# Kernel optimization log

Measured on AMD Instinct MI355X. Metric: run time of the kernel, lower is better.

Reference implementation:

```python
import jax, jax.numpy as jnp
import numpy as np

PARENT_LIST = [0, 0, 1, 2, 3, 4, 5, 6, 7, 8, 8, 3, 11, 12, 13, 14, 15, 15, 0, 18, 19, 20, 0, 22, 23, 24, 3]
J, D, H, L, DFF = 27, 512, 8, 6, 2048
DH = D // H
RADIUS = 0.1
B, N = 64, 2048
NEG = -1e9  # large finite negative: exp underflows to exactly 0 in fp32, grad-safe


def _topo_mask():
    m = np.full((J, J), NEG, dtype=np.float32)
    for c, p in enumerate(PARENT_LIST):
        m[c, c] = 0.0
        if c != p:
            m[c, p] = 0.0
            m[p, c] = 0.0
    return jnp.asarray(m)


def _radius_scales():
    s = np.ones(J, dtype=np.float32)
    s[[0, 1, 2, 3, 18, 22]] = 0.6
    s[[9, 10, 16, 17, 20, 21, 24, 25, 26]] = 1.5
    return jnp.asarray(s).reshape(1, J, 1)


def _ln(x, s, b):
    mu = jnp.mean(x, -1, keepdims=True)
    v = jnp.mean((x - mu) ** 2, -1, keepdims=True)
    return (x - mu) * jax.lax.rsqrt(v + 1e-5) * s + b


def _mha(q_in, k_in, v_in, qkv_w, qkv_b, out_w, out_b, add_mask):
    Bq, Q, _ = q_in.shape
    S = k_in.shape[1]
    q = (q_in @ qkv_w[:, :D] + qkv_b[:D]).reshape(Bq, Q, H, DH)
    k = (k_in @ qkv_w[:, D:2 * D] + qkv_b[D:2 * D]).reshape(Bq, S, H, DH)
    v = (v_in @ qkv_w[:, 2 * D:] + qkv_b[2 * D:]).reshape(Bq, S, H, DH)
    scores = jnp.einsum('bqhd,bkhd->bhqk', q, k) * np.float32(1.0 / np.sqrt(DH))
    attn = jax.nn.softmax(scores + add_mask, axis=-1)
    o = jnp.einsum('bhqk,bkhd->bqhd', attn, v).reshape(Bq, Q, D)
    return o @ out_w + out_b


def setup_inputs() -> dict:
    key = jax.random.key(0)
    ks = iter(jax.random.split(key, 40))
    def w(shape, scale=0.02):
        return jax.random.normal(next(ks), shape, jnp.float32) * scale
    return dict(
        x_t=jax.random.normal(next(ks), (B, J, 3), jnp.float32),
        t=jax.random.uniform(next(ks), (B, 1), jnp.float32),
        coarse_pose=jax.random.normal(next(ks), (B, J, 3), jnp.float32),
        radar_pc=jax.random.normal(next(ks), (B, N, 6), jnp.float32),
        pc_w=w((6, D)), pc_b=jnp.zeros(D),
        coarse_w=w((3, D)), coarse_b=jnp.zeros(D),
        state_w=w((3, D)), state_b=jnp.zeros(D),
        jid_emb=w((J, D), 1.0),
        dop_w1=w((1, 64)), dop_b1=jnp.zeros(64),
        dop_w2=w((64, D)), dop_b2=jnp.zeros(D),
        time_w1=w((1, D)), time_b1=jnp.zeros(D),
        time_w2=w((D, D)), time_b2=jnp.zeros(D),
        mod_w1=w((D, 2 * D)), mod_b1=jnp.zeros(2 * D),
        mod_w2=w((2 * D, 2 * D)), mod_b2=jnp.zeros(2 * D),
        diff_w=w((2 * D, D)), diff_b=jnp.zeros(D),
        vel_w=w((D, 3)), vel_b=jnp.zeros(3),
        sa_qkv_w=w((L, D, 3 * D)), sa_qkv_b=jnp.zeros((L, 3 * D)),
        sa_out_w=w((L, D, D)), sa_out_b=jnp.zeros((L, D)),
        ca_qkv_w=w((L, D, 3 * D)), ca_qkv_b=jnp.zeros((L, 3 * D)),
        ca_out_w=w((L, D, D)), ca_out_b=jnp.zeros((L, D)),
        ff1_w=w((L, D, DFF)), ff1_b=jnp.zeros((L, DFF)),
        ff2_w=w((L, DFF, D)), ff2_b=jnp.zeros((L, D)),
        ln1_s=jnp.ones((L, D)), ln1_b=jnp.zeros((L, D)),
        ln2_s=jnp.ones((L, D)), ln2_b=jnp.zeros((L, D)),
        ln3_s=jnp.ones((L, D)), ln3_b=jnp.zeros((L, D)),
    )


def reference(x_t, t, coarse_pose, radar_pc, pc_w, pc_b, coarse_w, coarse_b,
              state_w, state_b, jid_emb, dop_w1, dop_b1, dop_w2, dop_b2,
              time_w1, time_b1, time_w2, time_b2, mod_w1, mod_b1, mod_w2, mod_b2,
              diff_w, diff_b, vel_w, vel_b,
              sa_qkv_w, sa_qkv_b, sa_out_w, sa_out_b,
              ca_qkv_w, ca_qkv_b, ca_out_w, ca_out_b,
              ff1_w, ff1_b, ff2_w, ff2_b,
              ln1_s, ln1_b, ln2_s, ln2_b, ln3_s, ln3_b):
    p_idx = jnp.asarray(PARENT_LIST)
    topo = _topo_mask()          # [J,J] additive
    scales = _radius_scales()    # [1,J,1]
    pc_xyz = radar_pc[:, :, :3]
    pc_dop = radar_pc[:, :, 3:4]
    raw_memory = radar_pc @ pc_w + pc_b                               # [B,N,D]
    # euclidean distance via norm expansion (cdist p=2)
    d2 = (jnp.sum(x_t ** 2, -1)[:, :, None] + jnp.sum(pc_xyz ** 2, -1)[:, None, :]
          - 2.0 * jnp.einsum('bjc,bnc->bjn', x_t, pc_xyz))
    dist = jnp.sqrt(jnp.maximum(d2, 0.0))                             # [B,J,N]
    ar = scales * RADIUS                                              # [1,J,1]
    sig = ar / 2.0
    dw = jnp.exp(-dist ** 2 / (2.0 * sig ** 2))                       # [B,J,N]
    pi = jnp.max(dw, axis=1, keepdims=True)                           # [B,1,N]
    memory = raw_memory * jnp.swapaxes(pi, 1, 2)                      # [B,N,D]
    dop_feat = jax.nn.silu(pc_dop @ dop_w1 + dop_b1) @ dop_w2 + dop_b2
    denom = jnp.sum(dw, -1, keepdims=True) + 1e-6
    h_dop = jnp.einsum('bjn,bnd->bjd', dw, dop_feat) / denom
    h_coarse = coarse_pose @ coarse_w + coarse_b
    h_time = (jax.nn.silu(t @ time_w1 + time_b1) @ time_w2 + time_b2)[:, None, :]
    h_state = x_t @ state_w + state_b
    h_parent = h_state[:, p_idx, :]
    h_struct = jnp.concatenate([h_state, h_parent], -1) @ diff_w + diff_b
    query = h_coarse + h_time + h_dop + h_state + h_struct + jid_emb[None]
    mod = jax.nn.silu(h_state @ mod_w1 + mod_b1) @ mod_w2 + mod_b2
    shift, scale = jnp.split(mod, 2, axis=-1)
    query = query * (1.0 + scale) + shift
    # radius mask with nearest-point rescue
    smask = dist > ar
    min_idx = jnp.argmin(dist, axis=-1)                               # [B,J]
    rescue = jnp.arange(dist.shape[-1])[None, None, :] != min_idx[:, :, None]
    smask = jnp.where(jnp.all(smask, -1, keepdims=True), rescue, smask)
    mem_bias = jnp.where(smask, NEG, 0.0)[:, None, :, :]              # [B,1,J,N]
    tgt_bias = topo[None, None]                                       # [1,1,J,J]
    x = query
    for l in range(L):  # norm_first TransformerDecoderLayer, relu FFN, no dropout
        h = _ln(x, ln1_s[l], ln1_b[l])
        x = x + _mha(h, h, h, sa_qkv_w[l], sa_qkv_b[l], sa_out_w[l], sa_out_b[l], tgt_bias)
        h = _ln(x, ln2_s[l], ln2_b[l])
        x = x + _mha(h, memory, memory, ca_qkv_w[l], ca_qkv_b[l], ca_out_w[l], ca_out_b[l], mem_bias)
        h = _ln(x, ln3_s[l], ln3_b[l])
        x = x + jax.nn.relu(h @ ff1_w[l] + ff1_b[l]) @ ff2_w[l] + ff2_b[l]
    return x @ vel_w + vel_b
```

## Files before the change

kernel.cpp:

```cpp
#include <hip/hip_runtime.h>

#define J 27
#define D 512
#define H 8
#define DH 64
#define NLAYER 6
#define DFF 2048
#define NB 64
#define NP 2048
#define CAP 128
#define GCH 16
#define GPTS 128
#define NEGF -1000000000.0f

typedef unsigned short u16;
typedef __attribute__((ext_vector_type(8))) __bf16 bf16x8;
typedef __attribute__((ext_vector_type(4))) float f32x4;

__constant__ int c_parent[J] = {0,0,1,2,3,4,5,6,7,8,8,3,11,12,13,14,15,15,0,18,19,20,0,22,23,24,3};
__constant__ float c_scale[J] = {0.6f,0.6f,0.6f,0.6f,1.f,1.f,1.f,1.f,1.f,1.5f,1.5f,1.f,1.f,1.f,1.f,1.f,
                                 1.5f,1.5f,0.6f,1.f,1.5f,1.5f,0.6f,1.f,1.5f,1.5f,1.5f};

__device__ __forceinline__ float siluf(float x){ return x/(1.f+expf(-x)); }

__device__ __forceinline__ u16 f2bf(float f){
  union { float f; unsigned u; } x; x.f = f;
  unsigned r = x.u + 0x7FFFu + ((x.u >> 16) & 1u);
  return (u16)(r >> 16);
}
__device__ __forceinline__ float bf2f(u16 h){
  union { unsigned u; float f; } x; x.u = ((unsigned)h) << 16; return x.f;
}
__device__ __forceinline__ void csplit(float v, u16 &h, u16 &l){
  h = f2bf(v);
  l = f2bf(v - bf2f(h));
}

__global__ void k_perj(const float* __restrict__ x_t, const float* __restrict__ pc,
                       float* __restrict__ denom_sum, int* __restrict__ rescue,
                       int* __restrict__ allm, unsigned int* __restrict__ bitmap){
  int bj = blockIdx.x; int b = bj / J, j = bj % J;
  int t = threadIdx.x;
  float x0 = x_t[(b*J+j)*3+0];
  float x1 = x_t[(b*J+j)*3+1];
  float x2 = x_t[(b*J+j)*3+2];
  float sx = x0*x0+x1*x1+x2*x2;
  float ar = c_scale[j]*0.1f;
  float sig = ar*0.5f;
  float twos2 = 2.f*sig*sig;
  float sum = 0.f, bmin = 3.4e38f; int bidx = NP; int any = 0;
  for (int n = t; n < NP; n += 256){
    const float* p = pc + ((size_t)b*NP + n)*6;
    float p0=p[0], p1=p[1], p2=p[2];
    float d2 = sx + (p0*p0+p1*p1+p2*p2) - 2.f*(x0*p0+x1*p1+x2*p2);
    float dist = sqrtf(fmaxf(d2, 0.f));
    sum += expf(-(dist*dist)/twos2);
    if (dist < bmin){ bmin = dist; bidx = n; }
    if (dist <= ar){ any = 1; atomicOr(&bitmap[b*(NP/32)+(n>>5)], 1u<<(n&31)); }
// ... 37 lines not shown
      base++;
    }
  }
  if (t == 0) act_cnt[b] = total > CAP ? CAP : total;
}

__global__ void k_scan(const int* __restrict__ act_cnt, int* __restrict__ act_off,
                       int* __restrict__ act_total){
  if (threadIdx.x == 0){
    int s = 0;
    for (int b = 0; b < NB; ++b){ act_off[b] = s; s += act_cnt[b]; }
    act_total[0] = s;
  }
}

__launch_bounds__(256)
__global__ void k_gpart(const float* __restrict__ x_t, const float* __restrict__ pc,
                        const float* __restrict__ dop_w1, const float* __restrict__ dop_b1,
                        float* __restrict__ Gp){
  int b = blockIdx.x, ch = blockIdx.y; int t = threadIdx.x;
  __shared__ float sx[J*3];
  __shared__ float w1s[64], b1s[64];
  __shared__ float spx[GPTS], spy[GPTS], spz[GPTS], sdp[GPTS];
  __shared__ float hid[GPTS*65];
  __shared__ float dws[J*129];
  if (t < J*3) sx[t] = x_t[b*J*3 + t];
  if (t < 64){ w1s[t] = dop_w1[t]; b1s[t] = dop_b1[t]; }
  int n0 = ch*GPTS;
  if (t < GPTS){
    const float* p = pc + ((size_t)b*NP + n0 + t)*6;
    float2 f0 = *(const float2*)p;
    float2 f1 = *(const float2*)(p+2);
    spx[t]=f0.x; spy[t]=f0.y; spz[t]=f1.x; sdp[t]=f1.y;
  }
  __syncthreads();
  {
    int p = t>>1, h0 = (t&1)*32;
    float dop = sdp[p];
    #pragma unroll 8
    for (int i = 0; i < 32; ++i){
      int h = h0 + i;
      hid[p*65+h] = siluf(dop*w1s[h]+b1s[h]);
    }
  }
  for (int e = t; e < J*GPTS; e += 256){
    int j = e>>7, p = e&127;
    float x0=sx[j*3], x1=sx[j*3+1], x2=sx[j*3+2];
    float p0=spx[p], p1=spy[p], p2=spz[p];
    float d2 = (x0*x0+x1*x1+x2*x2) + (p0*p0+p1*p1+p2*p2) - 2.f*(x0*p0+x1*p1+x2*p2);
    float dist = sqrtf(fmaxf(d2, 0.f));
    float sig = c_scale[j]*0.05f;
    dws[j*129+p] = expf(-(dist*dist)/(2.f*sig*sig));
  }
  __syncthreads();
  int h = t & 63, jb = t >> 6;
  float acc[7] = {0.f,0.f,0.f,0.f,0.f,0.f,0.f};
  for (int p = 0; p < GPTS; ++p){
    float hv = hid[p*65+h];
    #pragma unroll
    for (int i = 0; i < 7; ++i){
      int j = jb + 4*i;
      if (j < J) acc[i] += dws[j*129+p]*hv;
    }
  }
  float* out = Gp + ((size_t)(b*GCH+ch))*J*64;
  #pragma unroll
  for (int i = 0; i < 7; ++i){
    int j = jb + 4*i;
    if (j < J) out[j*64+h] = acc[i];
  }
}

__global__ void k_gred(const float* __restrict__ Gp, float* __restrict__ G){
  int idx = blockIdx.x*256 + threadIdx.x;
  int bj = idx >> 6, h = idx & 63;
  int b = bj / J, j = bj % J;
  float s = 0.f;
  #pragma unroll
  for (int c = 0; c < GCH; ++c) s += Gp[((size_t)(b*GCH+c)*J + j)*64 + h];
  G[idx] = s;
}

__launch_bounds__(256)
__global__ void k_hdop2(const float* __restrict__ G, const float* __restrict__ dop_w2,
                        const float* __restrict__ dop_b2, const float* __restrict__ denom_sum,
                        float* __restrict__ h_dop){
  int b = blockIdx.x, half = blockIdx.y;
  int t = threadIdx.x;
  int d = half*256 + t;
  __shared__ float sG[J*64];
  __shared__ float sS[J], sI[J];
  for (int e = t; e < J*64; e += 256) sG[e] = G[(size_t)b*J*64 + e];
  if (t < J){ float S = denom_sum[b*J+t]; sS[t] = S; sI[t] = 1.f/(S+1e-6f); }
  __syncthreads();
  float acc[J];
  #pragma unroll
  for (int j = 0; j < J; ++j) acc[j] = 0.f;
  for (int h = 0; h < 64; ++h){
    float wv = dop_w2[h*D + d];
    #pragma unroll
    for (int j = 0; j < J; ++j) acc[j] += sG[j*64+h]*wv;
  }
  float b2 = dop_b2[d];
  #pragma unroll
  for (int j = 0; j < J; ++j)
    h_dop[(size_t)(b*J+j)*D + d] = (acc[j] + sS[j]*b2)*sI[j];
}

__global__ void k_stage1(const float* __restrict__ x_t, const float* __restrict__ state_w,
                         const float* __restrict__ state_b,
                         const float* __restrict__ coarse, const float* __restrict__ coarse_w,
                         const float* __restrict__ coarse_b,
                         const float* __restrict__ t_in, const float* __restrict__ time_w1,
                         const float* __restrict__ time_b1,
                         float* __restrict__ h_state, u16* __restrict__ hsh, u16* __restrict__ hsl,
                         float* __restrict__ h_coarse, u16* __restrict__ thh, u16* __restrict__ thl){
  const int RD = NB*J*D;
  int idx = blockIdx.x*256 + threadIdx.x;
  if (idx < RD){
    int r = idx / D, d = idx % D;
    const float* ir = x_t + r*3;
    float v = ir[0]*state_w[d] + ir[1]*state_w[D+d] + ir[2]*state_w[2*D+d] + state_b[d];
    h_state[idx] = v;
    u16 h,l; csplit(v,h,l); hsh[idx]=h; hsl[idx]=l;
  } else if (idx < 2*RD){
    int k = idx - RD;
    int r = k / D, d = k % D;
    const float* ir = coarse + r*3;
    h_coarse[k] = ir[0]*coarse_w[d] + ir[1]*coarse_w[D+d] + ir[2]*coarse_w[2*D+d] + coarse_b[d];
  } else if (idx < 2*RD + NB*D){
    int k = idx - 2*RD;
    int b = k / D, d = k % D;
    float v = siluf(t_in[b]*time_w1[d] + time_b1[d]);
    u16 h,l; csplit(v,h,l); thh[k]=h; thl[k]=l;
  }
}

__global__ void k_hs2(const float* __restrict__ h_state, u16* __restrict__ oh, u16* __restrict__ ol){
  int idx = blockIdx.x*256 + threadIdx.x;
  if (idx >= NB*J*2*D) return;
  int r = idx / (2*D), c = idx % (2*D);
  int b = r / J, j = r % J;
  float v;
  if (c < D) v = h_state[(size_t)r*D + c];
  else       v = h_state[((size_t)(b*J) + c_parent[j])*D + (c-D)];
  u16 h,l; csplit(v,h,l); oh[idx]=h; ol[idx]=l;
}

__global__ void k_query(const float* __restrict__ h_coarse, const float* __restrict__ h_time,
                        const float* __restrict__ h_dop, const float* __restrict__ h_state,
                        const float* __restrict__ hstruct, const float* __restrict__ jid,
                        const float* __restrict__ mod2, float* __restrict__ x){
  int idx = blockIdx.x*256 + threadIdx.x;
  if (idx >= NB*J*D) return;
  int r = idx / D, d = idx % D;
  int b = r / J, j = r % J;
  float q = h_coarse[idx] + h_time[b*D+d] + h_dop[idx] + h_state[idx] + hstruct[idx] + jid[j*D+d];
  float shift = mod2[(size_t)r*2*D + d];
  float scale = mod2[(size_t)r*2*D + D + d];
  x[idx] = q*(1.f+scale) + shift;
}

__global__ void k_memact(const float* __restrict__ x_t, const float* __restrict__ pc,
                         const float* __restrict__ pc_w, const float* __restrict__ pc_b,
                         const int* __restrict__ act_idx, const int* __restrict__ act_cnt,
                         const int* __restrict__ act_off, u16* __restrict__ mh, u16* __restrict__ ml){
  int b = blockIdx.x / CAP, i = blockIdx.x % CAP;
  if (i >= act_cnt[b]) return;
  int n = act_idx[b*CAP+i];
  int t = threadIdx.x;
  __shared__ float sdw[J];
  __shared__ float spi;
  const float* p = pc + ((size_t)b*NP+n)*6;
  if (t < J){
    float x0 = x_t[(b*J+t)*3+0], x1 = x_t[(b*J+t)*3+1], x2 = x_t[(b*J+t)*3+2];
    float p0=p[0], p1=p[1], p2=p[2];
    float d2 = (x0*x0+x1*x1+x2*x2) + (p0*p0+p1*p1+p2*p2) - 2.f*(x0*p0+x1*p1+x2*p2);
    float dist = sqrtf(fmaxf(d2,0.f));
    float sig = c_scale[t]*0.05f;
    sdw[t] = expf(-(dist*dist)/(2.f*sig*sig));
  }
  __syncthreads();
  if (t == 0){ float m = sdw[0]; for (int k = 1; k < J; ++k) m = fmaxf(m, sdw[k]); spi = m; }
  __syncthreads();
  float pi = spi;
  float p0=p[0],p1=p[1],p2=p[2],p3=p[3],p4=p[4],p5=p[5];
  int g = act_off[b] + i;
  for (int d = t; d < D; d += 128){
    float acc = pc_b[d] + p0*pc_w[d] + p1*pc_w[D+d] + p2*pc_w[2*D+d]
              + p3*pc_w[3*D+d] + p4*pc_w[4*D+d] + p5*pc_w[5*D+d];
    float v = acc * pi;
    u16 h,l; csplit(v,h,l);
    mh[(size_t)g*D + d] = h; ml[(size_t)g*D + d] = l;
  }
}

__launch_bounds__(256)
__global__ void k_wconv(const float* __restrict__ W, u16* __restrict__ Wt, int K, int N){
  int k0 = blockIdx.x*64, n0 = blockIdx.y*64;
  size_t zo = (size_t)blockIdx.z*K*N;
  __shared__ float tile[64][65];
  int t = threadIdx.x;
  #pragma unroll
  for (int i = 0; i < 16; ++i){
    int idx = i*256 + t; int k = idx>>6, n = idx&63;
    tile[k][n] = W[zo + (size_t)(k0+k)*N + n0+n];
  }
  __syncthreads();
  #pragma unroll
  for (int i = 0; i < 8; ++i){
    int idx = i*256 + t; int n = idx>>5, kp = (idx&31)*2;
    unsigned pk = (unsigned)f2bf(tile[kp][n]) | ((unsigned)f2bf(tile[kp+1][n])<<16);
    *(unsigned*)&Wt[zo + (size_t)(n0+n)*K + k0+kp] = pk;
  }
}

template<int TM>
__launch_bounds__(256)
__global__ void k_gemm(const u16* __restrict__ Agh, const u16* __restrict__ Agl,
                       const u16* __restrict__ Bt,
                       const float* __restrict__ bias, const float* __restrict__ res,
                       float* __restrict__ Cf, u16* __restrict__ Ch, u16* __restrict__ Cl,
                       int M, int N, int K, int act,
                       const int* __restrict__ Mdev, int ntx){
  int Meff = Mdev ? *Mdev : M;
  int nwg = gridDim.x;
  int q8 = nwg>>3, r8 = nwg&7;
  int xcd = blockIdx.x&7, loc = blockIdx.x>>3;
  int wg = (xcd < r8 ? xcd*(q8+1) : r8*(q8+1)+(xcd-r8)*q8) + loc;
  int row0 = (wg % ntx)*TM, col0 = (wg / ntx)*64;
  if (row0 >= Meff) return;

  constexpr int MFR = TM/32;
  constexpr int RW  = TM/2;
  __shared__ u16 sAh[TM*64], sAl[TM*64], sBh[64*64];
  int t = threadIdx.x;
  int lane = t&63, w = t>>6, wr = w>>1, wc = w&1;
  int sm = t>>3, kc = t&7;
  const u16* pAh1 = Agh + (size_t)(row0+sm)*K + kc*8;
  const u16* pAl1 = Agl + (size_t)(row0+sm)*K + kc*8;
  const u16* pAh2 = (TM==64) ? Agh + (size_t)(row0+sm+32)*K + kc*8 : pAh1;
  const u16* pAl2 = (TM==64) ? Agl + (size_t)(row0+sm+32)*K + kc*8 : pAl1;
  const u16* pB1 = Bt + (size_t)(col0+sm)*K + kc*8;
  const u16* pB2 = Bt + (size_t)(col0+sm+32)*K + kc*8;
  int o1 = (sm*128 + kc*16) ^ ((sm&7)<<4);
  int o2 = ((sm+32)*128 + kc*16) ^ ((sm&7)<<4);
  uint4 ra1, rl1, ra2, rl2, rb1, rb2;
  auto gload = [&](int kt){
    ra1 = *(const uint4*)(pAh1 + kt);
    rl1 = *(const uint4*)(pAl1 + kt);
    if constexpr (TM==64){
      ra2 = *(const uint4*)(pAh2 + kt);
      rl2 = *(const uint4*)(pAl2 + kt);
    }
    rb1 = *(const uint4*)(pB1 + kt);
    rb2 = *(const uint4*)(pB2 + kt);
  };
  auto stage = [&](){
    *(uint4*)((char*)sAh + o1) = ra1;
    *(uint4*)((char*)sAl + o1) = rl1;
    if constexpr (TM==64){
      *(uint4*)((char*)sAh + o2) = ra2;
      *(uint4*)((char*)sAl + o2) = rl2;
    }
    *(uint4*)((char*)sBh + o1) = rb1;
    *(uint4*)((char*)sBh + o2) = rb2;
  };
  int fr = lane&15, fkb = (lane>>4)*16;
  f32x4 acc[MFR][2] = {};
  gload(0);
  stage();
  __syncthreads();
  for (int kt = 0; kt < K; kt += 64){
    bool nxt = kt + 64 < K;
    if (nxt) gload(kt + 64);
    #pragma unroll
    for (int kk = 0; kk < 2; ++kk){
      bf16x8 ah[MFR], al[MFR], bh[2];
      #pragma unroll
      for (int m = 0; m < MFR; ++m){
        int row = wr*RW + m*16 + fr;
        int adr = (row*128 + kk*64 + fkb) ^ ((row&7)<<4);
        ah[m] = *(const bf16x8*)((char*)sAh + adr);
        al[m] = *(const bf16x8*)((char*)sAl + adr);
      }
      #pragma unroll
      for (int n = 0; n < 2; ++n){
        int rowb = wc*32 + n*16 + fr;
        int adr = (rowb*128 + kk*64 + fkb) ^ ((rowb&7)<<4);
        bh[n] = *(const bf16x8*)((char*)sBh + adr);
      }
      #pragma unroll
      for (int m = 0; m < MFR; ++m)
        #pragma unroll
        for (int n = 0; n < 2; ++n){
          acc[m][n] = __builtin_amdgcn_mfma_f32_16x16x32_bf16(al[m], bh[n], acc[m][n], 0,0,0);
          acc[m][n] = __builtin_amdgcn_mfma_f32_16x16x32_bf16(ah[m], bh[n], acc[m][n], 0,0,0);
        }
    }
    if (nxt){
      __syncthreads();
      stage();
      __syncthreads();
    }
  }
  int er = (lane>>4)*4, ec = lane&15;
  #pragma unroll
  for (int m = 0; m < MFR; ++m){
    #pragma unroll
    for (int qq = 0; qq < 4; ++qq){
      int r = row0 + wr*RW + m*16 + er + qq;
      if (r >= Meff) continue;
      #pragma unroll
      for (int n = 0; n < 2; ++n){
        int c = col0 + wc*32 + n*16 + ec;
        float v = acc[m][n][qq] + bias[c];
        if (res) v += res[(size_t)r*N + c];
        if (act == 1) v = v/(1.f+expf(-v));
        else if (act == 2) v = fmaxf(v, 0.f);
        if (Cf) Cf[(size_t)r*N + c] = v;
        if (Ch){
          u16 hh, ll; csplit(v, hh, ll);
          Ch[(size_t)r*N + c] = hh;
          Cl[(size_t)r*N + c] = ll;
        }
      }
    }
  }
}

__global__ void k_ln(const float* __restrict__ x, const float* __restrict__ s,
                     const float* __restrict__ bb, u16* __restrict__ oh, u16* __restrict__ ol){
  int r = blockIdx.x; int t = threadIdx.x;
  const float* xr = x + (size_t)r*D;
  float v0 = xr[t], v1 = xr[t+256];
  __shared__ float red[256];
  red[t] = v0+v1; __syncthreads();
  for (int st = 128; st > 0; st >>= 1){ if (t < st) red[t] += red[t+st]; __syncthreads(); }
  float mu = red[0]/(float)D;
  __syncthreads();
  float d0 = v0-mu, d1 = v1-mu;
  red[t] = d0*d0 + d1*d1; __syncthreads();
  for (int st = 128; st > 0; st >>= 1){ if (t < st) red[t] += red[t+st]; __syncthreads(); }
  float var = red[0]/(float)D;
  float rs = rsqrtf(var + 1e-5f);
  float y0 = d0*rs*s[t] + bb[t];
  float y1 = d1*rs*s[t+256] + bb[t+256];
  u16 h,l;
  csplit(y0,h,l); oh[(size_t)r*D+t]=h;     ol[(size_t)r*D+t]=l;
  csplit(y1,h,l); oh[(size_t)r*D+t+256]=h; ol[(size_t)r*D+t+256]=l;
}

__launch_bounds__(256)
__global__ void k_selfattn(const float* __restrict__ qkv, u16* __restrict__ oh, u16* __restrict__ ol){
  int bh = blockIdx.x; int b = bh / H, h = bh % H;
  int t = threadIdx.x;
  __shared__ float qs[J*DH], ks[J*DH], vs[J*DH];
  __shared__ float ss[J*J];
  for (int e = t; e < J*DH; e += 256){
    int j = e/DH, d = e%DH;
    const float* base = qkv + (size_t)(b*J+j)*1536 + h*DH + d;
    qs[e] = base[0]; ks[e] = base[512]; vs[e] = base[1024];
  }
  __syncthreads();
  for (int e = t; e < J*J; e += 256){
    int qj = e/J, kk = e%J;
    float acc = 0.f;
    for (int d = 0; d < DH; ++d) acc += qs[qj*DH+d]*ks[kk*DH+d];
    float bias = (qj==kk || c_parent[qj]==kk || c_parent[kk]==qj) ? 0.f : NEGF;
    ss[e] = acc*0.125f + bias;
  }
  __syncthreads();
  if (t < J){
    float m = -3.4e38f;
    for (int k = 0; k < J; ++k) m = fmaxf(m, ss[t*J+k]);
    float sum = 0.f;
    for (int k = 0; k < J; ++k){ float e_ = expf(ss[t*J+k]-m); ss[t*J+k] = e_; sum += e_; }
    float inv = 1.f/sum;
    for (int k = 0; k < J; ++k) ss[t*J+k] *= inv;
  }
  __syncthreads();
  for (int e = t; e < J*DH; e += 256){
    int j = e/DH, d = e%DH;
    float acc = 0.f;
    for (int k = 0; k < J; ++k) acc += ss[j*J+k]*vs[k*DH+d];
    u16 hh,ll; csplit(acc,hh,ll);
    oh[(size_t)(b*J+j)*D + h*DH + d] = hh;
    ol[(size_t)(b*J+j)*D + h*DH + d] = ll;
  }
}

__launch_bounds__(256)
__global__ void k_crossattn(const float* __restrict__ qbuf, const float* __restrict__ kv_act,
                            const float* __restrict__ x_t, const float* __restrict__ pc,
                            const int* __restrict__ act_idx, const int* __restrict__ act_cnt,
                            const int* __restrict__ act_off, const int* __restrict__ rescue,
                            const int* __restrict__ allm, u16* __restrict__ oh, u16* __restrict__ ol){
  int bh = blockIdx.x; int b = bh / H, h = bh % H;
  int t = threadIdx.x;
  int cnt = act_cnt[b], off = act_off[b];
  __shared__ float qs[J*DH];
  __shared__ float ks[CAP*DH];
  __shared__ float pxyz[CAP*3];
  __shared__ float sx[J*3];
  __shared__ int sn[CAP];
  __shared__ float ss[J*CAP];
  if (t < J*3) sx[t] = x_t[b*J*3+t];
  for (int e = t; e < J*DH; e += 256)
    qs[e] = qbuf[(size_t)(b*J + e/DH)*D + h*DH + (e%DH)];
  for (int e = t; e < cnt*DH; e += 256){
    int i = e/DH, d = e%DH;
    ks[e] = kv_act[(size_t)(off+i)*1024 + h*DH + d];
  }
  for (int i = t; i < cnt; i += 256){
    int n = act_idx[b*CAP+i]; sn[i] = n;
    const float* p = pc + ((size_t)b*NP+n)*6;
    pxyz[i*3] = p[0]; pxyz[i*3+1] = p[1]; pxyz[i*3+2] = p[2];
  }
  __syncthreads();
  for (int e = t; e < J*cnt; e += 256){
// ... 7 lines not shown
      float p0=pxyz[i*3], p1=pxyz[i*3+1], p2=pxyz[i*3+2];
      float d2 = (x0*x0+x1*x1+x2*x2) + (p0*p0+p1*p1+p2*p2) - 2.f*(x0*p0+x1*p1+x2*p2);
      float dist = sqrtf(fmaxf(d2,0.f));
      float ar = c_scale[j]*0.1f;
      bias = (dist > ar) ? NEGF : 0.f;
    }
    ss[j*CAP+i] = acc*0.125f + bias;
  }
  __syncthreads();
  if (t < J){
    float m = -3.4e38f;
    for (int i = 0; i < cnt; ++i) m = fmaxf(m, ss[t*CAP+i]);
    float sum = 0.f;
    for (int i = 0; i < cnt; ++i){ float e_ = expf(ss[t*CAP+i]-m); ss[t*CAP+i] = e_; sum += e_; }
    float inv = 1.f/sum;
    for (int i = 0; i < cnt; ++i) ss[t*CAP+i] *= inv;
  }
  __syncthreads();
  for (int e = t; e < J*DH; e += 256){
    int j = e/DH, d = e%DH;
    float acc = 0.f;
    for (int i = 0; i < cnt; ++i)
      acc += ss[j*CAP+i]*kv_act[(size_t)(off+i)*1024 + 512 + h*DH + d];
    u16 hh,ll; csplit(acc,hh,ll);
    oh[(size_t)(b*J+j)*D + h*DH + d] = hh;
    ol[(size_t)(b*J+j)*D + h*DH + d] = ll;
  }
}

__global__ void k_vel(const float* __restrict__ x, const float* __restrict__ vel_w,
                      const float* __restrict__ vel_b, float* __restrict__ out){
  int r = blockIdx.x; int t = threadIdx.x;
  int c = t >> 6; int lane = t & 63;
  float acc = 0.f;
  const float* xr = x + (size_t)r*D;
  for (int d = lane; d < D; d += 64) acc += xr[d]*vel_w[d*3+c];
  for (int s = 32; s > 0; s >>= 1) acc += __shfl_down(acc, s);
  if (lane == 0) out[r*3+c] = acc + vel_b[c];
}

static void gemm(const u16* Ah, const u16* Al, const u16* Bt, const float* bias,
                 const float* res, float* Cf, u16* Ch, u16* Cl,
                 int M, int N, int K, int act, const int* Mdev, int tm, hipStream_t s){
  if (tm == 32){
    int ntx = (M + 31) / 32;
    k_gemm<32><<<ntx*(N/64), 256, 0, s>>>(Ah, Al, Bt, bias, res, Cf, Ch, Cl, M, N, K, act, Mdev, ntx);
  } else {
    int ntx = (M + 63) / 64;
    k_gemm<64><<<ntx*(N/64), 256, 0, s>>>(Ah, Al, Bt, bias, res, Cf, Ch, Cl, M, N, K, act, Mdev, ntx);
  }
}

extern "C" void kernel_launch(void* const* d_in, const int* in_sizes, int n_in,
                              void* d_out, int out_size, void* d_ws, size_t ws_size,
                              hipStream_t stream){
  const float* x_t        = (const float*)d_in[0];
  const float* t_in       = (const float*)d_in[1];
  const float* coarse     = (const float*)d_in[2];
  const float* radar      = (const float*)d_in[3];
  const float* pc_w       = (const float*)d_in[4];
  const float* pc_b       = (const float*)d_in[5];
  const float* coarse_w   = (const float*)d_in[6];
  const float* coarse_b   = (const float*)d_in[7];
  const float* state_w    = (const float*)d_in[8];
  const float* state_b    = (const float*)d_in[9];
  const float* jid_emb    = (const float*)d_in[10];
  const float* dop_w1     = (const float*)d_in[11];
  const float* dop_b1     = (const float*)d_in[12];
  const float* dop_w2     = (const float*)d_in[13];
  const float* dop_b2     = (const float*)d_in[14];
  const float* time_w1    = (const float*)d_in[15];
  const float* time_b1    = (const float*)d_in[16];
// ... 36 lines not shown
    return r;
  };
  float*        denom_sum = (float*)alloc(R*4);
  int*          rescue    = (int*)  alloc(R*4);
  int*          allm      = (int*)  alloc(R*4);
  unsigned int* bitmap    = (unsigned int*)alloc(NB*(NP/32)*4);
  int*          act_idx   = (int*)  alloc(NB*CAP*4);
  int*          act_cnt   = (int*)  alloc(NB*4);
  int*          act_off   = (int*)  alloc(NB*4);
  int*          act_total = (int*)  alloc(64);
  float* Gp       = (float*)alloc((size_t)NB*GCH*J*64*4);
  float* G        = (float*)alloc((size_t)R*64*4);
  float* h_dop    = (float*)alloc((size_t)R*D*4);
  float* h_state  = (float*)alloc((size_t)R*D*4);
  float* h_coarse = (float*)alloc((size_t)R*D*4);
  float* hstruct  = (float*)alloc((size_t)R*D*4);
  float* xres     = (float*)alloc((size_t)R*D*4);
  float* qbuf     = (float*)alloc((size_t)R*D*4);
  float* h_time   = (float*)alloc((size_t)NB*D*4);
  float* mod2     = (float*)alloc((size_t)R*2*D*4);
  float* qkv      = (float*)alloc((size_t)R*3*D*4);
  float* kv_act   = (float*)alloc((size_t)NB*CAP*2*D*4);
  u16* hsh   = (u16*)alloc((size_t)R*D*2);
  u16* hsl   = (u16*)alloc((size_t)R*D*2);
  u16* hbufh = (u16*)alloc((size_t)R*D*2);
  u16* hbufl = (u16*)alloc((size_t)R*D*2);
  u16* attnoh= (u16*)alloc((size_t)R*D*2);
  u16* attnol= (u16*)alloc((size_t)R*D*2);
  u16* ffhh  = (u16*)alloc((size_t)R*DFF*2);
  u16* ffhl  = (u16*)alloc((size_t)R*DFF*2);
  u16* mah   = (u16*)alloc((size_t)NB*CAP*D*2);
  u16* mal   = (u16*)alloc((size_t)NB*CAP*D*2);
  u16* time_w2t = (u16*)alloc((size_t)512*512*2);
  u16* mod_w1t  = (u16*)alloc((size_t)1024*512*2);
  u16* mod_w2t  = (u16*)alloc((size_t)1024*1024*2);
  u16* diff_wt  = (u16*)alloc((size_t)512*1024*2);
  u16* sa_qkv_t = (u16*)alloc((size_t)NLAYER*1536*512*2);
  u16* sa_out_t = (u16*)alloc((size_t)NLAYER*512*512*2);
  u16* ca_qkv_t = (u16*)alloc((size_t)NLAYER*1536*512*2);
  u16* ca_out_t = (u16*)alloc((size_t)NLAYER*512*512*2);
  u16* ff1_t    = (u16*)alloc((size_t)NLAYER*2048*512*2);
  u16* ff2_t    = (u16*)alloc((size_t)NLAYER*512*2048*2);
  u16* thh   = attnoh;
  u16* thl   = attnol;
  u16* mod1h = ffhh;
  u16* mod1l = ffhl;
  u16* hs2h  = (u16*)kv_act;
  u16* hs2l  = (u16*)kv_act + (size_t)R*2*D;

  k_wconv<<<dim3(8, 8, 1),  256, 0, stream>>>(time_w2, time_w2t, 512, 512);
  k_wconv<<<dim3(8, 16, 1), 256, 0, stream>>>(mod_w1, mod_w1t, 512, 1024);
  k_wconv<<<dim3(16, 16, 1),256, 0, stream>>>(mod_w2, mod_w2t, 1024, 1024);
  k_wconv<<<dim3(16, 8, 1), 256, 0, stream>>>(diff_w, diff_wt, 1024, 512);
  k_wconv<<<dim3(8, 24, NLAYER), 256, 0, stream>>>(sa_qkv_w, sa_qkv_t, 512, 1536);
  k_wconv<<<dim3(8, 8, NLAYER),  256, 0, stream>>>(sa_out_w, sa_out_t, 512, 512);
  k_wconv<<<dim3(8, 24, NLAYER), 256, 0, stream>>>(ca_qkv_w, ca_qkv_t, 512, 1536);
  k_wconv<<<dim3(8, 8, NLAYER),  256, 0, stream>>>(ca_out_w, ca_out_t, 512, 512);
  k_wconv<<<dim3(8, 32, NLAYER), 256, 0, stream>>>(ff1_w, ff1_t, 512, 2048);
  k_wconv<<<dim3(32, 8, NLAYER), 256, 0, stream>>>(ff2_w, ff2_t, 2048, 512);

  hipMemsetAsync(bitmap, 0, NB*(NP/32)*4, stream);
  k_perj<<<R, 256, 0, stream>>>(x_t, radar, denom_sum, rescue, allm, bitmap);
  k_compact<<<NB, 64, 0, stream>>>(bitmap, act_idx, act_cnt);
  k_scan<<<1, 64, 0, stream>>>(act_cnt, act_off, act_total);
  k_gpart<<<dim3(NB, GCH), 256, 0, stream>>>(x_t, radar, dop_w1, dop_b1, Gp);
  k_gred<<<R*64/256, 256, 0, stream>>>(Gp, G);
  k_hdop2<<<dim3(NB, 2), 256, 0, stream>>>(G, dop_w2, dop_b2, denom_sum, h_dop);

  k_stage1<<<(2*R*D + NB*D + 255)/256, 256, 0, stream>>>(
      x_t, state_w, state_b, coarse, coarse_w, coarse_b, t_in, time_w1, time_b1,
      h_state, hsh, hsl, h_coarse, thh, thl);
  gemm(thh, thl, time_w2t, time_b2, nullptr, h_time, nullptr, nullptr, NB, 512, 512, 0, nullptr, 32, stream);
  gemm(hsh, hsl, mod_w1t, mod_b1, nullptr, nullptr, mod1h, mod1l, R, 1024, 512, 1, nullptr, 32, stream);
  gemm(mod1h, mod1l, mod_w2t, mod_b2, nullptr, mod2, nullptr, nullptr, R, 1024, 1024, 0, nullptr, 32, stream);
  k_hs2<<<(R*2*D+255)/256, 256, 0, stream>>>(h_state, hs2h, hs2l);
  gemm(hs2h, hs2l, diff_wt, diff_b, nullptr, hstruct, nullptr, nullptr, R, 512, 1024, 0, nullptr, 32, stream);
  k_query<<<(R*D+255)/256, 256, 0, stream>>>(h_coarse, h_time, h_dop, h_state, hstruct,
                                             jid_emb, mod2, xres);
  k_memact<<<NB*CAP, 128, 0, stream>>>(x_t, radar, pc_w, pc_b, act_idx, act_cnt, act_off, mah, mal);

  for (int l = 0; l < NLAYER; ++l){
    k_ln<<<R, 256, 0, stream>>>(xres, ln1_s + l*D, ln1_b + l*D, hbufh, hbufl);
    gemm(hbufh, hbufl, sa_qkv_t + (size_t)l*1536*512, sa_qkv_b + l*1536, nullptr,
         qkv, nullptr, nullptr, R, 1536, 512, 0, nullptr, 32, stream);
    k_selfattn<<<NB*H, 256, 0, stream>>>(qkv, attnoh, attnol);
    gemm(attnoh, attnol, sa_out_t + (size_t)l*512*512, sa_out_b + l*D, xres,
         xres, nullptr, nullptr, R, 512, 512, 0, nullptr, 32, stream);

    k_ln<<<R, 256, 0, stream>>>(xres, ln2_s + l*D, ln2_b + l*D, hbufh, hbufl);
    gemm(hbufh, hbufl, ca_qkv_t + (size_t)l*1536*512, ca_qkv_b + l*1536, nullptr,
         qbuf, nullptr, nullptr, R, 512, 512, 0, nullptr, 32, stream);
    gemm(mah, mal, ca_qkv_t + (size_t)l*1536*512 + (size_t)512*512, ca_qkv_b + l*1536 + 512,
         nullptr, kv_act, nullptr, nullptr, NB*CAP, 1024, 512, 0, act_total, 64, stream);
    k_crossattn<<<NB*H, 256, 0, stream>>>(qbuf, kv_act, x_t, radar, act_idx, act_cnt,
                                          act_off, rescue, allm, attnoh, attnol);
    gemm(attnoh, attnol, ca_out_t + (size_t)l*512*512, ca_out_b + l*D, xres,
         xres, nullptr, nullptr, R, 512, 512, 0, nullptr, 32, stream);

    k_ln<<<R, 256, 0, stream>>>(xres, ln3_s + l*D, ln3_b + l*D, hbufh, hbufl);
    gemm(hbufh, hbufl, ff1_t + (size_t)l*2048*512, ff1_b + l*DFF, nullptr,
         nullptr, ffhh, ffhl, R, 2048, 512, 2, nullptr, 32, stream);
    gemm(ffhh, ffhl, ff2_t + (size_t)l*512*2048, ff2_b + l*D, xres,
         xres, nullptr, nullptr, R, 512, 2048, 0, nullptr, 32, stream);
  }

  k_vel<<<R, 192, 0, stream>>>(xres, vel_w, vel_b, (float*)d_out);
}
```

Measured before the change: 1.217 ms.

## Drop split-bf16 activation compensation and use MFMA for doppler reduction

Activations were previously split into high and low bf16 halves, and every GEMM ran two MFMAs per tile to recover near-fp32 accuracy. This change keeps only the single bf16 value, which halves A-operand loads, shared memory and MFMA count, and removes the low-part buffers. The doppler weighted-sum kernel is also rewritten to use bf16 MFMA on swizzled shared tiles instead of a scalar FMA loop. Accuracy drops to plain bf16 for activations and for the Gaussian weights.

```diff
diff --git a/kernel.cpp b/kernel.cpp
--- a/kernel.cpp
+++ b/kernel.cpp
@@ -27,13 +27,6 @@
   union { float f; unsigned u; } x; x.f = f;
   unsigned r = x.u + 0x7FFFu + ((x.u >> 16) & 1u);
   return (u16)(r >> 16);
-}
-__device__ __forceinline__ float bf2f(u16 h){
-  union { unsigned u; float f; } x; x.u = ((unsigned)h) << 16; return x.f;
-}
-__device__ __forceinline__ void csplit(float v, u16 &h, u16 &l){
-  h = f2bf(v);
-  l = f2bf(v - bf2f(h));
 }
 
 __global__ void k_perj(const float* __restrict__ x_t, const float* __restrict__ pc,
@@ -117,8 +110,8 @@
   __shared__ float sx[J*3];
   __shared__ float w1s[64], b1s[64];
   __shared__ float spx[GPTS], spy[GPTS], spz[GPTS], sdp[GPTS];
-  __shared__ float hid[GPTS*65];
-  __shared__ float dws[J*129];
+  __shared__ u16 hidT[64*128];
+  __shared__ u16 dwsA[32*128];
   if (t < J*3) sx[t] = x_t[b*J*3 + t];
   if (t < 64){ w1s[t] = dop_w1[t]; b1s[t] = dop_b1[t]; }
   int n0 = ch*GPTS;
@@ -130,39 +123,73 @@
   }
   __syncthreads();
   {
-    int p = t>>1, h0 = (t&1)*32;
-    float dop = sdp[p];
-    #pragma unroll 8
-    for (int i = 0; i < 32; ++i){
-      int h = h0 + i;
-      hid[p*65+h] = siluf(dop*w1s[h]+b1s[h]);
-    }
-  }
-  for (int e = t; e < J*GPTS; e += 256){
-    int j = e>>7, p = e&127;
-    float x0=sx[j*3], x1=sx[j*3+1], x2=sx[j*3+2];
-    float p0=spx[p], p1=spy[p], p2=spz[p];
-    float d2 = (x0*x0+x1*x1+x2*x2) + (p0*p0+p1*p1+p2*p2) - 2.f*(x0*p0+x1*p1+x2*p2);
-    float dist = sqrtf(fmaxf(d2, 0.f));
-    float sig = c_scale[j]*0.05f;
-    dws[j*129+p] = expf(-(dist*dist)/(2.f*sig*sig));
-  }
-  __syncthreads();
-  int h = t & 63, jb = t >> 6;
-  float acc[7] = {0.f,0.f,0.f,0.f,0.f,0.f,0.f};
-  for (int p = 0; p < GPTS; ++p){
-    float hv = hid[p*65+h];
+    int h = t & 63, pb = (t>>6)*32;
+    float w1 = w1s[h], b1 = b1s[h];
+    char* base = (char*)hidT;
     #pragma unroll
-    for (int i = 0; i < 7; ++i){
-      int j = jb + 4*i;
-      if (j < J) acc[i] += dws[j*129+p]*hv;
+    for (int m = 0; m < 16; ++m){
+      float v0 = siluf(sdp[pb+2*m]*w1 + b1);
+      float v1 = siluf(sdp[pb+2*m+1]*w1 + b1);
+      unsigned pk = (unsigned)f2bf(v0) | ((unsigned)f2bf(v1) << 16);
+      int off = (h*256 + pb*2 + 4*m) ^ ((h&7)<<4);
+      *(unsigned*)(base + off) = pk;
+    }
+  }
+  {
+    int j = t & 31, pb = (t>>5)*16;
+    if (j < J){
+      float x0=sx[j*3], x1=sx[j*3+1], x2=sx[j*3+2];
+      float sxx = x0*x0+x1*x1+x2*x2;
+      float sig = c_scale[j]*0.05f;
+      float inv2 = 1.f/(2.f*sig*sig);
+      char* base = (char*)dwsA;
+      #pragma unroll
+      for (int m = 0; m < 8; ++m){
+        float v[2];
+        #pragma unroll
+        for (int u = 0; u < 2; ++u){
+          int p = pb + 2*m + u;
+          float p0=spx[p], p1=spy[p], p2=spz[p];
+          float d2 = sxx + (p0*p0+p1*p1+p2*p2) - 2.f*(x0*p0+x1*p1+x2*p2);
+          float dist = sqrtf(fmaxf(d2, 0.f));
+          v[u] = expf(-(dist*dist)*inv2);
+        }
+        unsigned pk = (unsigned)f2bf(v[0]) | ((unsigned)f2bf(v[1]) << 16);
+        int off = (j*256 + pb*2 + 4*m) ^ ((j&7)<<4);
+        *(unsigned*)(base + off) = pk;
+      }
+    }
+  }
+  __syncthreads();
+  int lane = t & 63, wv = t >> 6;
+  int h0 = wv * 16;
+  int fr = lane & 15, fkb = (lane>>4)*16;
+  f32x4 acc[2] = {};
+  #pragma unroll
+  for (int ks = 0; ks < 4; ++ks){
+    bf16x8 bfrag;
+    {
+      int row = h0 + fr;
+      int adr = (row*256 + ks*64 + fkb) ^ ((row&7)<<4);
+      bfrag = *(const bf16x8*)((char*)hidT + adr);
+    }
+    #pragma unroll
+    for (int m = 0; m < 2; ++m){
+      int row = m*16 + fr;
+      int adr = (row*256 + ks*64 + fkb) ^ ((row&7)<<4);
+      bf16x8 afrag = *(const bf16x8*)((char*)dwsA + adr);
+      acc[m] = __builtin_amdgcn_mfma_f32_16x16x32_bf16(afrag, bfrag, acc[m], 0,0,0);
     }
   }
   float* out = Gp + ((size_t)(b*GCH+ch))*J*64;
+  int er = (lane>>4)*4, ec = lane&15;
   #pragma unroll
-  for (int i = 0; i < 7; ++i){
-    int j = jb + 4*i;
-    if (j < J) out[j*64+h] = acc[i];
+  for (int m = 0; m < 2; ++m){
+    #pragma unroll
+    for (int q = 0; q < 4; ++q){
+      int j = m*16 + er + q;
+      if (j < J) out[j*64 + h0 + ec] = acc[m][q];
+    }
   }
 }
 
@@ -208,8 +235,8 @@
                          const float* __restrict__ coarse_b,
                          const float* __restrict__ t_in, const float* __restrict__ time_w1,
                          const float* __restrict__ time_b1,
-                         float* __restrict__ h_state, u16* __restrict__ hsh, u16* __restrict__ hsl,
-                         float* __restrict__ h_coarse, u16* __restrict__ thh, u16* __restrict__ thl){
+                         float* __restrict__ h_state, u16* __restrict__ hsh,
+                         float* __restrict__ h_coarse, u16* __restrict__ thh){
   const int RD = NB*J*D;
   int idx = blockIdx.x*256 + threadIdx.x;
   if (idx < RD){
@@ -217,7 +244,7 @@
     const float* ir = x_t + r*3;
     float v = ir[0]*state_w[d] + ir[1]*state_w[D+d] + ir[2]*state_w[2*D+d] + state_b[d];
     h_state[idx] = v;
-    u16 h,l; csplit(v,h,l); hsh[idx]=h; hsl[idx]=l;
+    hsh[idx] = f2bf(v);
   } else if (idx < 2*RD){
     int k = idx - RD;
     int r = k / D, d = k % D;
@@ -227,11 +254,11 @@
     int k = idx - 2*RD;
     int b = k / D, d = k % D;
     float v = siluf(t_in[b]*time_w1[d] + time_b1[d]);
-    u16 h,l; csplit(v,h,l); thh[k]=h; thl[k]=l;
-  }
-}
-
-__global__ void k_hs2(const float* __restrict__ h_state, u16* __restrict__ oh, u16* __restrict__ ol){
+    thh[k] = f2bf(v);
+  }
+}
+
+__global__ void k_hs2(const float* __restrict__ h_state, u16* __restrict__ oh){
   int idx = blockIdx.x*256 + threadIdx.x;
   if (idx >= NB*J*2*D) return;
   int r = idx / (2*D), c = idx % (2*D);
@@ -239,7 +266,7 @@
   float v;
   if (c < D) v = h_state[(size_t)r*D + c];
   else       v = h_state[((size_t)(b*J) + c_parent[j])*D + (c-D)];
-  u16 h,l; csplit(v,h,l); oh[idx]=h; ol[idx]=l;
+  oh[idx] = f2bf(v);
 }
 
 __global__ void k_query(const float* __restrict__ h_coarse, const float* __restrict__ h_time,
@@ -259,7 +286,7 @@
 __global__ void k_memact(const float* __restrict__ x_t, const float* __restrict__ pc,
                          const float* __restrict__ pc_w, const float* __restrict__ pc_b,
                          const int* __restrict__ act_idx, const int* __restrict__ act_cnt,
-                         const int* __restrict__ act_off, u16* __restrict__ mh, u16* __restrict__ ml){
+                         const int* __restrict__ act_off, u16* __restrict__ mh){
   int b = blockIdx.x / CAP, i = blockIdx.x % CAP;
   if (i >= act_cnt[b]) return;
   int n = act_idx[b*CAP+i];
@@ -284,9 +311,7 @@
   for (int d = t; d < D; d += 128){
     float acc = pc_b[d] + p0*pc_w[d] + p1*pc_w[D+d] + p2*pc_w[2*D+d]
               + p3*pc_w[3*D+d] + p4*pc_w[4*D+d] + p5*pc_w[5*D+d];
-    float v = acc * pi;
-    u16 h,l; csplit(v,h,l);
-    mh[(size_t)g*D + d] = h; ml[(size_t)g*D + d] = l;
+    mh[(size_t)g*D + d] = f2bf(acc * pi);
   }
 }
 
@@ -312,10 +337,9 @@
 
 template<int TM>
 __launch_bounds__(256)
-__global__ void k_gemm(const u16* __restrict__ Agh, const u16* __restrict__ Agl,
-                       const u16* __restrict__ Bt,
+__global__ void k_gemm(const u16* __restrict__ Ag, const u16* __restrict__ Bt,
                        const float* __restrict__ bias, const float* __restrict__ res,
-                       float* __restrict__ Cf, u16* __restrict__ Ch, u16* __restrict__ Cl,
+                       float* __restrict__ Cf, u16* __restrict__ Ch,
                        int M, int N, int K, int act,
                        const int* __restrict__ Mdev, int ntx){
   int Meff = Mdev ? *Mdev : M;
@@ -328,38 +352,28 @@
 
   constexpr int MFR = TM/32;
   constexpr int RW  = TM/2;
-  __shared__ u16 sAh[TM*64], sAl[TM*64], sBh[64*64];
+  __shared__ u16 sA[TM*64], sB[64*64];
   int t = threadIdx.x;
   int lane = t&63, w = t>>6, wr = w>>1, wc = w&1;
   int sm = t>>3, kc = t&7;
-  const u16* pAh1 = Agh + (size_t)(row0+sm)*K + kc*8;
-  const u16* pAl1 = Agl + (size_t)(row0+sm)*K + kc*8;
-  const u16* pAh2 = (TM==64) ? Agh + (size_t)(row0+sm+32)*K + kc*8 : pAh1;
-  const u16* pAl2 = (TM==64) ? Agl + (size_t)(row0+sm+32)*K + kc*8 : pAl1;
+  const u16* pA1 = Ag + (size_t)(row0+sm)*K + kc*8;
+  const u16* pA2 = (TM==64) ? Ag + (size_t)(row0+sm+32)*K + kc*8 : pA1;
   const u16* pB1 = Bt + (size_t)(col0+sm)*K + kc*8;
   const u16* pB2 = Bt + (size_t)(col0+sm+32)*K + kc*8;
   int o1 = (sm*128 + kc*16) ^ ((sm&7)<<4);
   int o2 = ((sm+32)*128 + kc*16) ^ ((sm&7)<<4);
-  uint4 ra1, rl1, ra2, rl2, rb1, rb2;
+  uint4 ra1, ra2, rb1, rb2;
   auto gload = [&](int kt){
-    ra1 = *(const uint4*)(pAh1 + kt);
-    rl1 = *(const uint4*)(pAl1 + kt);
-    if constexpr (TM==64){
-      ra2 = *(const uint4*)(pAh2 + kt);
-      rl2 = *(const uint4*)(pAl2 + kt);
-    }
+    ra1 = *(const uint4*)(pA1 + kt);
+    if constexpr (TM==64) ra2 = *(const uint4*)(pA2 + kt);
     rb1 = *(const uint4*)(pB1 + kt);
     rb2 = *(const uint4*)(pB2 + kt);
   };
   auto stage = [&](){
-    *(uint4*)((char*)sAh + o1) = ra1;
-    *(uint4*)((char*)sAl + o1) = rl1;
-    if constexpr (TM==64){
-      *(uint4*)((char*)sAh + o2) = ra2;
-      *(uint4*)((char*)sAl + o2) = rl2;
-    }
-    *(uint4*)((char*)sBh + o1) = rb1;
-    *(uint4*)((char*)sBh + o2) = rb2;
+    *(uint4*)((char*)sA + o1) = ra1;
+    if constexpr (TM==64) *(uint4*)((char*)sA + o2) = ra2;
+    *(uint4*)((char*)sB + o1) = rb1;
+    *(uint4*)((char*)sB + o2) = rb2;
   };
   int fr = lane&15, fkb = (lane>>4)*16;
   f32x4 acc[MFR][2] = {};
@@ -371,27 +385,24 @@
     if (nxt) gload(kt + 64);
     #pragma unroll
     for (int kk = 0; kk < 2; ++kk){
-      bf16x8 ah[MFR], al[MFR], bh[2];
+      bf16x8 af[MFR], bf[2];
       #pragma unroll
       for (int m = 0; m < MFR; ++m){
         int row = wr*RW + m*16 + fr;
         int adr = (row*128 + kk*64 + fkb) ^ ((row&7)<<4);
-        ah[m] = *(const bf16x8*)((char*)sAh + adr);
-        al[m] = *(const bf16x8*)((char*)sAl + adr);
+        af[m] = *(const bf16x8*)((char*)sA + adr);
       }
       #pragma unroll
       for (int n = 0; n < 2; ++n){
         int rowb = wc*32 + n*16 + fr;
         int adr = (rowb*128 + kk*64 + fkb) ^ ((rowb&7)<<4);
-        bh[n] = *(const bf16x8*)((char*)sBh + adr);
+        bf[n] = *(const bf16x8*)((char*)sB + adr);
       }
       #pragma unroll
       for (int m = 0; m < MFR; ++m)
         #pragma unroll
-        for (int n = 0; n < 2; ++n){
-          acc[m][n] = __builtin_amdgcn_mfma_f32_16x16x32_bf16(al[m], bh[n], acc[m][n], 0,0,0);
-          acc[m][n] = __builtin_amdgcn_mfma_f32_16x16x32_bf16(ah[m], bh[n], acc[m][n], 0,0,0);
-        }
+        for (int n = 0; n < 2; ++n)
+          acc[m][n] = __builtin_amdgcn_mfma_f32_16x16x32_bf16(af[m], bf[n], acc[m][n], 0,0,0);
     }
     if (nxt){
       __syncthreads();
@@ -414,18 +425,14 @@
         if (act == 1) v = v/(1.f+expf(-v));
         else if (act == 2) v = fmaxf(v, 0.f);
         if (Cf) Cf[(size_t)r*N + c] = v;
-        if (Ch){
-          u16 hh, ll; csplit(v, hh, ll);
-          Ch[(size_t)r*N + c] = hh;
-          Cl[(size_t)r*N + c] = ll;
-        }
+        if (Ch) Ch[(size_t)r*N + c] = f2bf(v);
       }
     }
   }
 }
 
 __global__ void k_ln(const float* __restrict__ x, const float* __restrict__ s,
-                     const float* __restrict__ bb, u16* __restrict__ oh, u16* __restrict__ ol){
+                     const float* __restrict__ bb, u16* __restrict__ oh){
   int r = blockIdx.x; int t = threadIdx.x;
   const float* xr = x + (size_t)r*D;
   float v0 = xr[t], v1 = xr[t+256];
@@ -439,15 +446,12 @@
   for (int st = 128; st > 0; st >>= 1){ if (t < st) red[t] += red[t+st]; __syncthreads(); }
   float var = red[0]/(float)D;
   float rs = rsqrtf(var + 1e-5f);
-  float y0 = d0*rs*s[t] + bb[t];
-  float y1 = d1*rs*s[t+256] + bb[t+256];
-  u16 h,l;
-  csplit(y0,h,l); oh[(size_t)r*D+t]=h;     ol[(size_t)r*D+t]=l;
-  csplit(y1,h,l); oh[(size_t)r*D+t+256]=h; ol[(size_t)r*D+t+256]=l;
+  oh[(size_t)r*D + t]       = f2bf(d0*rs*s[t]       + bb[t]);
+  oh[(size_t)r*D + t + 256] = f2bf(d1*rs*s[t+256]   + bb[t+256]);
 }
 
 __launch_bounds__(256)
-__global__ void k_selfattn(const float* __restrict__ qkv, u16* __restrict__ oh, u16* __restrict__ ol){
+__global__ void k_selfattn(const float* __restrict__ qkv, u16* __restrict__ oh){
   int bh = blockIdx.x; int b = bh / H, h = bh % H;
   int t = threadIdx.x;
   __shared__ float qs[J*DH], ks[J*DH], vs[J*DH];
@@ -479,9 +483,7 @@
     int j = e/DH, d = e%DH;
     float acc = 0.f;
     for (int k = 0; k < J; ++k) acc += ss[j*J+k]*vs[k*DH+d];
-    u16 hh,ll; csplit(acc,hh,ll);
-    oh[(size_t)(b*J+j)*D + h*DH + d] = hh;
-    ol[(size_t)(b*J+j)*D + h*DH + d] = ll;
+    oh[(size_t)(b*J+j)*D + h*DH + d] = f2bf(acc);
   }
 }
 
@@ -490,7 +492,7 @@
                             const float* __restrict__ x_t, const float* __restrict__ pc,
                             const int* __restrict__ act_idx, const int* __restrict__ act_cnt,
                             const int* __restrict__ act_off, const int* __restrict__ rescue,
-                            const int* __restrict__ allm, u16* __restrict__ oh, u16* __restrict__ ol){
+                            const int* __restrict__ allm, u16* __restrict__ oh){
   int bh = blockIdx.x; int b = bh / H, h = bh % H;
   int t = threadIdx.x;
   int cnt = act_cnt[b], off = act_off[b];
@@ -544,9 +546,7 @@
     float acc = 0.f;
     for (int i = 0; i < cnt; ++i)
       acc += ss[j*CAP+i]*kv_act[(size_t)(off+i)*1024 + 512 + h*DH + d];
-    u16 hh,ll; csplit(acc,hh,ll);
-    oh[(size_t)(b*J+j)*D + h*DH + d] = hh;
-    ol[(size_t)(b*J+j)*D + h*DH + d] = ll;
+    oh[(size_t)(b*J+j)*D + h*DH + d] = f2bf(acc);
   }
 }
 
@@ -561,15 +561,15 @@
   if (lane == 0) out[r*3+c] = acc + vel_b[c];
 }
 
-static void gemm(const u16* Ah, const u16* Al, const u16* Bt, const float* bias,
-                 const float* res, float* Cf, u16* Ch, u16* Cl,
+static void gemm(const u16* Ah, const u16* Bt, const float* bias,
+                 const float* res, float* Cf, u16* Ch,
                  int M, int N, int K, int act, const int* Mdev, int tm, hipStream_t s){
   if (tm == 32){
     int ntx = (M + 31) / 32;
-    k_gemm<32><<<ntx*(N/64), 256, 0, s>>>(Ah, Al, Bt, bias, res, Cf, Ch, Cl, M, N, K, act, Mdev, ntx);
+    k_gemm<32><<<ntx*(N/64), 256, 0, s>>>(Ah, Bt, bias, res, Cf, Ch, M, N, K, act, Mdev, ntx);
   } else {
     int ntx = (M + 63) / 64;
-    k_gemm<64><<<ntx*(N/64), 256, 0, s>>>(Ah, Al, Bt, bias, res, Cf, Ch, Cl, M, N, K, act, Mdev, ntx);
+    k_gemm<64><<<ntx*(N/64), 256, 0, s>>>(Ah, Bt, bias, res, Cf, Ch, M, N, K, act, Mdev, ntx);
   }
 }
 
@@ -652,15 +652,10 @@
   float* qkv      = (float*)alloc((size_t)R*3*D*4);
   float* kv_act   = (float*)alloc((size_t)NB*CAP*2*D*4);
   u16* hsh   = (u16*)alloc((size_t)R*D*2);
-  u16* hsl   = (u16*)alloc((size_t)R*D*2);
   u16* hbufh = (u16*)alloc((size_t)R*D*2);
-  u16* hbufl = (u16*)alloc((size_t)R*D*2);
   u16* attnoh= (u16*)alloc((size_t)R*D*2);
-  u16* attnol= (u16*)alloc((size_t)R*D*2);
   u16* ffhh  = (u16*)alloc((size_t)R*DFF*2);
-  u16* ffhl  = (u16*)alloc((size_t)R*DFF*2);
   u16* mah   = (u16*)alloc((size_t)NB*CAP*D*2);
-  u16* mal   = (u16*)alloc((size_t)NB*CAP*D*2);
   u16* time_w2t = (u16*)alloc((size_t)512*512*2);
   u16* mod_w1t  = (u16*)alloc((size_t)1024*512*2);
   u16* mod_w2t  = (u16*)alloc((size_t)1024*1024*2);
@@ -672,11 +667,8 @@
   u16* ff1_t    = (u16*)alloc((size_t)NLAYER*2048*512*2);
   u16* ff2_t    = (u16*)alloc((size_t)NLAYER*512*2048*2);
   u16* thh   = attnoh;
-  u16* thl   = attnol;
   u16* mod1h = ffhh;
-  u16* mod1l = ffhl;
   u16* hs2h  = (u16*)kv_act;
-  u16* hs2l  = (u16*)kv_act + (size_t)R*2*D;
 
   k_wconv<<<dim3(8, 8, 1),  256, 0, stream>>>(time_w2, time_w2t, 512, 512);
   k_wconv<<<dim3(8, 16, 1), 256, 0, stream>>>(mod_w1, mod_w1t, 512, 1024);
@@ -699,39 +691,39 @@
 
   k_stage1<<<(2*R*D + NB*D + 255)/256, 256, 0, stream>>>(
       x_t, state_w, state_b, coarse, coarse_w, coarse_b, t_in, time_w1, time_b1,
-      h_state, hsh, hsl, h_coarse, thh, thl);
-  gemm(thh, thl, time_w2t, time_b2, nullptr, h_time, nullptr, nullptr, NB, 512, 512, 0, nullptr, 32, stream);
-  gemm(hsh, hsl, mod_w1t, mod_b1, nullptr, nullptr, mod1h, mod1l, R, 1024, 512, 1, nullptr, 32, stream);
-  gemm(mod1h, mod1l, mod_w2t, mod_b2, nullptr, mod2, nullptr, nullptr, R, 1024, 1024, 0, nullptr, 32, stream);
-  k_hs2<<<(R*2*D+255)/256, 256, 0, stream>>>(h_state, hs2h, hs2l);
-  gemm(hs2h, hs2l, diff_wt, diff_b, nullptr, hstruct, nullptr, nullptr, R, 512, 1024, 0, nullptr, 32, stream);
+      h_state, hsh, h_coarse, thh);
+  gemm(thh, time_w2t, time_b2, nullptr, h_time, nullptr, NB, 512, 512, 0, nullptr, 32, stream);
+  gemm(hsh, mod_w1t, mod_b1, nullptr, nullptr, mod1h, R, 1024, 512, 1, nullptr, 32, stream);
+  gemm(mod1h, mod_w2t, mod_b2, nullptr, mod2, nullptr, R, 1024, 1024, 0, nullptr, 32, stream);
+  k_hs2<<<(R*2*D+255)/256, 256, 0, stream>>>(h_state, hs2h);
+  gemm(hs2h, diff_wt, diff_b, nullptr, hstruct, nullptr, R, 512, 1024, 0, nullptr, 32, stream);
   k_query<<<(R*D+255)/256, 256, 0, stream>>>(h_coarse, h_time, h_dop, h_state, hstruct,
                                              jid_emb, mod2, xres);
-  k_memact<<<NB*CAP, 128, 0, stream>>>(x_t, radar, pc_w, pc_b, act_idx, act_cnt, act_off, mah, mal);
+  k_memact<<<NB*CAP, 128, 0, stream>>>(x_t, radar, pc_w, pc_b, act_idx, act_cnt, act_off, mah);
 
   for (int l = 0; l < NLAYER; ++l){
-    k_ln<<<R, 256, 0, stream>>>(xres, ln1_s + l*D, ln1_b + l*D, hbufh, hbufl);
-    gemm(hbufh, hbufl, sa_qkv_t + (size_t)l*1536*512, sa_qkv_b + l*1536, nullptr,
-         qkv, nullptr, nullptr, R, 1536, 512, 0, nullptr, 32, stream);
-    k_selfattn<<<NB*H, 256, 0, stream>>>(qkv, attnoh, attnol);
-    gemm(attnoh, attnol, sa_out_t + (size_t)l*512*512, sa_out_b + l*D, xres,
-         xres, nullptr, nullptr, R, 512, 512, 0, nullptr, 32, stream);
-
-    k_ln<<<R, 256, 0, stream>>>(xres, ln2_s + l*D, ln2_b + l*D, hbufh, hbufl);
-    gemm(hbufh, hbufl, ca_qkv_t + (size_t)l*1536*512, ca_qkv_b + l*1536, nullptr,
-         qbuf, nullptr, nullptr, R, 512, 512, 0, nullptr, 32, stream);
-    gemm(mah, mal, ca_qkv_t + (size_t)l*1536*512 + (size_t)512*512, ca_qkv_b + l*1536 + 512,
-         nullptr, kv_act, nullptr, nullptr, NB*CAP, 1024, 512, 0, act_total, 64, stream);
+    k_ln<<<R, 256, 0, stream>>>(xres, ln1_s + l*D, ln1_b + l*D, hbufh);
+    gemm(hbufh, sa_qkv_t + (size_t)l*1536*512, sa_qkv_b + l*1536, nullptr,
+         qkv, nullptr, R, 1536, 512, 0, nullptr, 32, stream);
+    k_selfattn<<<NB*H, 256, 0, stream>>>(qkv, attnoh);
+    gemm(attnoh, sa_out_t + (size_t)l*512*512, sa_out_b + l*D, xres,
+         xres, nullptr, R, 512, 512, 0, nullptr, 32, stream);
+
+    k_ln<<<R, 256, 0, stream>>>(xres, ln2_s + l*D, ln2_b + l*D, hbufh);
+    gemm(hbufh, ca_qkv_t + (size_t)l*1536*512, ca_qkv_b + l*1536, nullptr,
+         qbuf, nullptr, R, 512, 512, 0, nullptr, 32, stream);
+    gemm(mah, ca_qkv_t + (size_t)l*1536*512 + (size_t)512*512, ca_qkv_b + l*1536 + 512,
+         nullptr, kv_act, nullptr, NB*CAP, 1024, 512, 0, act_total, 64, stream);
     k_crossattn<<<NB*H, 256, 0, stream>>>(qbuf, kv_act, x_t, radar, act_idx, act_cnt,
-                                          act_off, rescue, allm, attnoh, attnol);
-    gemm(attnoh, attnol, ca_out_t + (size_t)l*512*512, ca_out_b + l*D, xres,
-         xres, nullptr, nullptr, R, 512, 512, 0, nullptr, 32, stream);
-
-    k_ln<<<R, 256, 0, stream>>>(xres, ln3_s + l*D, ln3_b + l*D, hbufh, hbufl);
-    gemm(hbufh, hbufl, ff1_t + (size_t)l*2048*512, ff1_b + l*DFF, nullptr,
-         nullptr, ffhh, ffhl, R, 2048, 512, 2, nullptr, 32, stream);
-    gemm(ffhh, ffhl, ff2_t + (size_t)l*512*2048, ff2_b + l*D, xres,
-         xres, nullptr, nullptr, R, 512, 2048, 0, nullptr, 32, stream);
+                                          act_off, rescue, allm, attnoh);
+    gemm(attnoh, ca_out_t + (size_t)l*512*512, ca_out_b + l*D, xres,
+         xres, nullptr, R, 512, 512, 0, nullptr, 32, stream);
+
+    k_ln<<<R, 256, 0, stream>>>(xres, ln3_s + l*D, ln3_b + l*D, hbufh);
+    gemm(hbufh, ff1_t + (size_t)l*2048*512, ff1_b + l*DFF, nullptr,
+         nullptr, ffhh, R, 2048, 512, 2, nullptr, 32, stream);
+    gemm(ffhh, ff2_t + (size_t)l*512*2048, ff2_b + l*D, xres,
+         xres, nullptr, R, 512, 2048, 0, nullptr, 32, stream);
   }
 
   k_vel<<<R, 192, 0, stream>>>(xres, vel_w, vel_b, (float*)d_out);
```

Measured after the change: 1.062 ms. 1.15x faster.
